# Optimization experiments

Hardware: AMD Instinct MI355X
Metric: run time of the kernel (lower is better)

The kernel has to match this reference:

```python
import jax, jax.numpy as jnp
import numpy as np
import math

B, CH, BINS, W = 2, 8, 1024, 1024
FF = 2048
BANDS = 4
HD = BINS // BANDS
EPS = 1e-5


def _ln(x, g, b):
    m = jnp.mean(x, -1, keepdims=True)
    v = jnp.mean(jnp.square(x - m), -1, keepdims=True)
    return (x - m) * jax.lax.rsqrt(v + EPS) * g + b


def _conv1d(x, w, pad, groups=1):
    # x: [B, C, W], w: [O, I/groups, k]
    return jax.lax.conv_general_dilated(x, w, (1,), [(pad, pad)],
                                        dimension_numbers=('NCH', 'OIH', 'NCH'),
                                        feature_group_count=groups)


def _attn(h, mem, qw, qb, qcw, qcb, kw, kb, kcw, kcb, vw, vb, vcw, vcb, ow, ob, er):
    b, w, c = h.shape

    def proj(src, lw, lb, cw, cb):
        y = src @ lw.T + lb                                   # [b, w, c]
        y = _conv1d(y.transpose(0, 2, 1), cw, 1, groups=c) + cb[None, :, None]
        return y.transpose(0, 2, 1)                           # [b, w, c]

    q = proj(h, qw, qb, qcw, qcb).reshape(b, w, BANDS, HD).transpose(0, 2, 1, 3)   # [b, n, w, hd]
    k = proj(mem, kw, kb, kcw, kcb).reshape(b, w, BANDS, HD).transpose(0, 2, 1, 3)
    v = proj(mem, vw, vb, vcw, vcb).reshape(b, w, BANDS, HD).transpose(0, 2, 1, 3)
    # relative position bias via Music-Transformer pad/skew trick
    p = jnp.einsum('bnwh,hc->bnwc', q, er)                    # [b, n, w, W]
    p = jnp.pad(p, ((0, 0), (0, 0), (0, 0), (1, 0))).transpose(0, 1, 3, 2)[:, :, 1:, :]
    qk = (jnp.einsum('bnqh,bnkh->bnqk', q, k) + p) / math.sqrt(c)
    a = jax.nn.softmax(qk, axis=-1)
    o = jnp.einsum('bnqk,bnkh->bnqh', a, v).transpose(0, 2, 1, 3).reshape(b, w, c)
    return o @ ow.T + ob


def _forward(x, w_in, ln1_g, ln1_b, glu_w, ln2_g, ln2_b, c1L_w, c1R_w, ln3_g, ln3_b,
             c1M_dw, c1M_pw, ln4_g, ln4_b, qw, qb, qcw, qcb, kw, kb, kcw, kcb,
             vw, vb, vcw, vcb, ow, ob, er, ln5_g, ln5_b, c2_w, c3_w):
    # in_project: Linear(channels, 1, bias=False) on x.transpose(1,3), squeeze
    xf = jnp.einsum('bcfw,c->bwf', x, w_in)                   # [B, W, BINS]
    # GLU block
    h = _ln(xf, ln1_g, ln1_b)
    g = h @ glu_w.T
    ga, gb = jnp.split(g, 2, axis=-1)
    xf = xf + ga * jax.nn.sigmoid(gb)
    # conv feedforward block
    h = _ln(xf, ln2_g, ln2_b)
    hL = jax.nn.relu(h @ c1L_w.T)                             # [B, W, FF]
    hR = jax.nn.relu(_conv1d(h.transpose(0, 2, 1), c1R_w, 1)).transpose(0, 2, 1)  # [B, W, FF//4]
    hR = jnp.pad(hR, ((0, 0), (0, 0), (0, FF - FF // 4)))
    h = _ln(hL + hR, ln3_g, ln3_b)
    h = _conv1d(_conv1d(h.transpose(0, 2, 1), c1M_dw, 4, groups=FF), c1M_pw, 0).transpose(0, 2, 1)
    xf = xf + h
    # multiband attention
    h = _ln(xf, ln4_g, ln4_b)
    h = _attn(h, h, qw, qb, qcw, qcb, kw, kb, kcw, kcb, vw, vb, vcw, vcb, ow, ob, er)
    xf = xf + h
    # squared-relu FFN
    h = _ln(xf, ln5_g, ln5_b)
    h = jnp.square(jax.nn.relu(h @ c2_w.T)) @ c3_w.T
    xf = xf + h
    return xf.transpose(0, 2, 1)[:, None, :, :]               # [B, 1, BINS, W]


def setup_inputs() -> dict:
    key = jax.random.key(0)
    keys = iter(jax.random.split(key, 48))

    def n(shape, s=0.02):
        return jax.random.normal(next(keys), shape, dtype=jnp.float32) * s

    ones = lambda d: jnp.ones((d,), jnp.float32)
    zeros = lambda d: jnp.zeros((d,), jnp.float32)
    return {
        'x': jax.random.normal(next(keys), (B, CH, BINS, W), dtype=jnp.float32),
        'w_in': n((CH,)),
        'ln1_g': ones(BINS), 'ln1_b': zeros(BINS),
        'glu_w': n((2 * BINS, BINS)),
        'ln2_g': ones(BINS), 'ln2_b': zeros(BINS),
        'c1L_w': n((FF, BINS)),
        'c1R_w': n((FF // 4, BINS, 3)),
        'ln3_g': ones(FF), 'ln3_b': zeros(FF),
        'c1M_dw': n((FF, 1, 9)),
        'c1M_pw': n((BINS, FF, 1)),
        'ln4_g': ones(BINS), 'ln4_b': zeros(BINS),
        'qw': n((BINS, BINS)), 'qb': zeros(BINS), 'qcw': n((BINS, 1, 3)), 'qcb': zeros(BINS),
        'kw': n((BINS, BINS)), 'kb': zeros(BINS), 'kcw': n((BINS, 1, 3)), 'kcb': zeros(BINS),
        'vw': n((BINS, BINS)), 'vb': zeros(BINS), 'vcw': n((BINS, 1, 3)), 'vcb': zeros(BINS),
        'ow': n((BINS, BINS)), 'ob': zeros(BINS),
        'er': n((HD, W), s=1.0),
        'ln5_g': ones(BINS), 'ln5_b': zeros(BINS),
        'c2_w': n((FF, BINS)), 'c3_w': n((BINS, FF)),
    }


def reference(x, w_in, ln1_g, ln1_b, glu_w, ln2_g, ln2_b, c1L_w, c1R_w, ln3_g, ln3_b,
              c1M_dw, c1M_pw, ln4_g, ln4_b, qw, qb, qcw, qcb, kw, kb, kcw, kcb,
              vw, vb, vcw, vcb, ow, ob, er, ln5_g, ln5_b, c2_w, c3_w):
    return _forward(x, w_in, ln1_g, ln1_b, glu_w, ln2_g, ln2_b, c1L_w, c1R_w, ln3_g, ln3_b,
                    c1M_dw, c1M_pw, ln4_g, ln4_b, qw, qb, qcw, qcb, kw, kb, kcw, kcb,
                    vw, vb, vcw, vcb, ow, ob, er, ln5_g, ln5_b, c2_w, c3_w)
```

## Files before the change

kernel.cpp:

```cpp
#include <hip/hip_runtime.h>


typedef float f32x4 __attribute__((ext_vector_type(4)));
typedef short short8 __attribute__((ext_vector_type(8)));
typedef unsigned short u16;
typedef unsigned int u32;

__device__ __forceinline__ float bf2f(u16 u){
  u32 v = ((u32)u) << 16;
  return __builtin_bit_cast(float, v);
}
__device__ __forceinline__ u16 f2bf(float f){
  u32 u = __builtin_bit_cast(u32, f);
  u32 r = (u + 0x7fffu + ((u >> 16) & 1u)) >> 16;
  return (u16)r;
}
__device__ __forceinline__ u32 pack2(float a, float b){
  return (u32)f2bf(a) | ((u32)f2bf(b) << 16);
}
__device__ __forceinline__ void unpack8(uint4 u, float* f){
  f[0]=bf2f(u.x & 0xffffu); f[1]=bf2f(u.x >> 16);
  f[2]=bf2f(u.y & 0xffffu); f[3]=bf2f(u.y >> 16);
  f[4]=bf2f(u.z & 0xffffu); f[5]=bf2f(u.z >> 16);
  f[6]=bf2f(u.w & 0xffffu); f[7]=bf2f(u.w >> 16);
}

__device__ __forceinline__ void gload16(const u16* g, u16* l){
  __builtin_amdgcn_global_load_lds(
      (const __attribute__((address_space(1))) unsigned int*)g,
      (__attribute__((address_space(3))) unsigned int*)l, 16, 0, 0);
}
template<int N> __device__ __forceinline__ void waitvm(){
  asm volatile("s_waitcnt vmcnt(%0)" :: "n"(N) : "memory");
}
__device__ __forceinline__ void barrier(){ __builtin_amdgcn_s_barrier(); }

template<int ACT, int OB, int MR, int NR, int DUAL, int NBUF, int RB, int SC>
__global__ __launch_bounds__(256)
void gemm_bt(const u16* __restrict__ A, const u16* __restrict__ Bw,
             const u16* __restrict__ A2, const u16* __restrict__ B2,
             float* __restrict__ Cf, u16* __restrict__ Cb,
             const float* __restrict__ bias, const void* __restrict__ resid,
             int M, int N, int K, int K2,
             int lda, int ldb, int lda2, int ldb2, int ldc,
             int apad, int aoff,
             long aZHi, long aZLo, long bZHi, long bZLo,
             long b2ZHi, long b2ZLo, long cZHi, long cZLo)
{
  constexpr int BM = 32 * MR, BN = 32 * NR;
  constexpr int LPT = MR + NR;
  constexpr int PRE = NBUF - 1;
  __shared__ __align__(16) u16 As[NBUF][BM * 64];
  __shared__ __align__(16) u16 Bs[NBUF][BN * 64];
  const int z = blockIdx.z, zh = z >> 2, zl = z & 3;
  const u16* Az = A + zh * aZHi + zl * aZLo;
  const u16* Bz = Bw + zh * bZHi + zl * bZLo;
  const u16* B2z = DUAL ? (B2 + zh * b2ZHi + zl * b2ZLo) : nullptr;
  const long coff = (long)zh * cZHi + (long)zl * cZLo;
  const int tid = threadIdx.x;
  const int m0 = blockIdx.y * BM, n0 = blockIdx.x * BN;
  const int lane = tid & 63, wid = tid >> 6;
  const int wm = wid >> 1, wn = wid & 1;
  const int lr = lane & 15, lk = lane >> 4;
  const int kA = K >> 6;
  const int NT = kA + (DUAL ? (K2 >> 6) : 0);

  auto stage = [&](int buf, int s){
    #pragma unroll
    for (int i = 0; i < MR; i++){
      int ch = tid + i * 256;
      int r = ch >> 3, c = ch & 7;
      int csw = (c ^ (r & 7)) * 8;
      const u16* src;
      bool d2 = DUAL && (s >= kA);
      if (d2){
        src = A2 + (long)(m0 + r) * lda2 + (s - kA) * 64 + csw;
      } else {
        int gm = m0 + r;
        long ar = (long)gm + (long)(gm >> 10) * apad + aoff;
        src = Az + ar * lda + s * 64 + csw;
      }
      gload16(src, &As[buf][ch * 8]);
    }
    #pragma unroll
    for (int i = 0; i < NR; i++){
      int ch = tid + i * 256;
      int r = ch >> 3, c = ch & 7;
      int csw = (c ^ (r & 7)) * 8;
      const u16* src;
      bool d2 = DUAL && (s >= kA);
      if (d2) src = B2z + (long)(n0 + r) * ldb2 + (s - kA) * 64 + csw;
      else    src = Bz  + (long)(n0 + r) * ldb  + s * 64 + csw;
      gload16(src, &Bs[buf][ch * 8]);
    }
  };

  f32x4 acc[MR][NR];
  #pragma unroll
  for (int i = 0; i < MR; i++)
    #pragma unroll
    for (int j = 0; j < NR; j++) acc[i][j] = f32x4{0.f, 0.f, 0.f, 0.f};

  auto compute = [&](int cur){
    const u16* Ab = &As[cur][0];
    const u16* Bb = &Bs[cur][0];
    short8 av[2][MR], bv[2][NR];
    #pragma unroll
    for (int h = 0; h < 2; h++){
      int g = h * 4 + lk;
      #pragma unroll
      for (int i = 0; i < MR; i++){
        int row = wm * 16 * MR + i * 16 + lr;
        av[h][i] = *(const short8*)(Ab + row * 64 + ((g ^ (row & 7)) * 8));
      }
      #pragma unroll
      for (int j = 0; j < NR; j++){
        int row = wn * 16 * NR + j * 16 + lr;
        bv[h][j] = *(const short8*)(Bb + row * 64 + ((g ^ (row & 7)) * 8));
      }
    }
    #pragma unroll
    for (int h = 0; h < 2; h++)
      #pragma unroll
      for (int i = 0; i < MR; i++)
        #pragma unroll
        for (int j = 0; j < NR; j++)
          acc[i][j] = __builtin_amdgcn_mfma_f32_16x16x32_bf16(av[h][i], bv[h][j], acc[i][j], 0, 0, 0);
  };

  const int npre = NT < PRE ? NT : PRE;
  for (int p = 0; p < npre; p++) stage(p, p);
  int s = 0;
  for (; s < NT - PRE; s++){
    waitvm<(NBUF - 2) * LPT>();
    barrier();
    stage((s + PRE) % NBUF, s + PRE);
    compute(s % NBUF);
    barrier();
  }
  for (; s < NT; s++){
    waitvm<0>();
    barrier();
    compute(s % NBUF);
    barrier();
  }

  float* CfZ = Cf ? Cf + coff : nullptr;
  u16*  CbZ = Cb ? Cb + coff : nullptr;
  const float* rzf = (!RB && resid) ? ((const float*)resid) + coff : nullptr;
  const u16*  rzb = (RB && resid) ? ((const u16*)resid) + coff : nullptr;
  #pragma unroll
  for (int i = 0; i < MR; i++){
    int rowb = m0 + wm * 16 * MR + i * 16 + lk * 4;
    #pragma unroll
    for (int j = 0; j < NR; j++){
      int colg = n0 + wn * 16 * NR + j * 16 + lr;
      f32x4 v = acc[i][j];
      float bvl = bias ? bias[colg] : 0.f;
      #pragma unroll
      for (int r = 0; r < 4; r++){
        long idx = (long)(rowb + r) * ldc + colg;
        float xv = v[r] + bvl;
        if constexpr (ACT == 1){ xv = fmaxf(xv, 0.f); }
        if constexpr (ACT == 2){ xv = fmaxf(xv, 0.f); xv = xv * xv; }
        if constexpr (SC){ xv *= 0.03125f; }
        if constexpr (RB){ if (rzb) xv += bf2f(rzb[idx]); }
        else             { if (rzf) xv += rzf[idx]; }
        if constexpr (OB) CbZ[idx] = f2bf(xv); else CfZ[idx] = xv;
      }
    }
  }
}

template<int NBUF>
__global__ __launch_bounds__(256)
void gemm_glu(const u16* __restrict__ A, const u16* __restrict__ Bw,
              u16* __restrict__ XF)
{
  constexpr int LPT = 6;
  constexpr int PRE = NBUF - 1;
  constexpr int NT = 16;
  __shared__ __align__(16) u16 As[NBUF][64 * 64];
  __shared__ __align__(16) u16 Bs[NBUF][128 * 64];
  const int tid = threadIdx.x;
  const int m0 = blockIdx.y * 64, n0 = blockIdx.x * 64;
  const int lane = tid & 63, wid = tid >> 6;
  const int wm = wid >> 1, wn = wid & 1;
  const int lr = lane & 15, lk = lane >> 4;

  auto stage = [&](int buf, int s){
    #pragma unroll
    for (int i = 0; i < 2; i++){
      int ch = tid + i * 256;
      int r = ch >> 3, c = ch & 7;
      int csw = (c ^ (r & 7)) * 8;
      gload16(A + (long)(m0 + r) * 1024 + s * 64 + csw, &As[buf][ch * 8]);
    }
    #pragma unroll
    for (int i = 0; i < 4; i++){
      int ch = tid + i * 256;
      int r = ch >> 3, c = ch & 7;
      int csw = (c ^ (r & 7)) * 8;
      int grow = (r < 64) ? (n0 + r) : (1024 + n0 + r - 64);
      gload16(Bw + (long)grow * 1024 + s * 64 + csw, &Bs[buf][ch * 8]);
    }
  };

  f32x4 accv[2][2], accg[2][2];
  #pragma unroll
  for (int i = 0; i < 2; i++)
    #pragma unroll
    for (int j = 0; j < 2; j++){
      accv[i][j] = f32x4{0.f,0.f,0.f,0.f};
      accg[i][j] = f32x4{0.f,0.f,0.f,0.f};
    }

  auto compute = [&](int cur){
    const u16* Ab = &As[cur][0];
    const u16* Bb = &Bs[cur][0];
    short8 av[2][2], bvv[2][2], bvg[2][2];
    #pragma unroll
    for (int h = 0; h < 2; h++){
      int g = h * 4 + lk;
      #pragma unroll
      for (int i = 0; i < 2; i++){
        int row = wm * 32 + i * 16 + lr;
        av[h][i] = *(const short8*)(Ab + row * 64 + ((g ^ (row & 7)) * 8));
      }
      #pragma unroll
      for (int j = 0; j < 2; j++){
        int row = wn * 32 + j * 16 + lr;
        bvv[h][j] = *(const short8*)(Bb + row * 64 + ((g ^ (row & 7)) * 8));
        int rowg = 64 + row;
        bvg[h][j] = *(const short8*)(Bb + rowg * 64 + ((g ^ (rowg & 7)) * 8));
      }
    }
    #pragma unroll
    for (int h = 0; h < 2; h++)
      #pragma unroll
      for (int i = 0; i < 2; i++)
        #pragma unroll
        for (int j = 0; j < 2; j++){
          accv[i][j] = __builtin_amdgcn_mfma_f32_16x16x32_bf16(av[h][i], bvv[h][j], accv[i][j], 0, 0, 0);
          accg[i][j] = __builtin_amdgcn_mfma_f32_16x16x32_bf16(av[h][i], bvg[h][j], accg[i][j], 0, 0, 0);
        }
  };

  const int npre = NT < PRE ? NT : PRE;
  for (int p = 0; p < npre; p++) stage(p, p);
  int s = 0;
  for (; s < NT - PRE; s++){
    waitvm<(NBUF - 2) * LPT>();
    barrier();
    stage((s + PRE) % NBUF, s + PRE);
    compute(s % NBUF);
    barrier();
  }
  for (; s < NT; s++){
    waitvm<0>();
    barrier();
    compute(s % NBUF);
    barrier();
  }

  #pragma unroll
  for (int i = 0; i < 2; i++){
    int rowb = m0 + wm * 32 + i * 16 + lk * 4;
    #pragma unroll
    for (int j = 0; j < 2; j++){
      int colg = n0 + wn * 32 + j * 16 + lr;
      #pragma unroll
      for (int r = 0; r < 4; r++){
        long idx = (long)(rowb + r) * 1024 + colg;
        float g = accg[i][j][r];
        float nv = bf2f(XF[idx]) + accv[i][j][r] / (1.f + __expf(-g));
        XF[idx] = f2bf(nv);
      }
    }
  }
}

template<int NC, int INBF>
__global__ __launch_bounds__(256)
void ln_kernel(const void* __restrict__ in, u16* __restrict__ out,
               const float* __restrict__ gg, const float* __restrict__ bb,
               int rowpad, int rowadd)
{
  constexpr int PER = NC / 256;
  const int row = blockIdx.x;
  const int tid = threadIdx.x;
  float v[PER];
  if constexpr (INBF){
    const u16* x = ((const u16*)in) + (long)row * NC + tid * PER;
    if constexpr (PER == 4){
      uint2 u = *(const uint2*)x;
      v[0]=bf2f(u.x & 0xffffu); v[1]=bf2f(u.x >> 16);
      v[2]=bf2f(u.y & 0xffffu); v[3]=bf2f(u.y >> 16);
    } else {
      #pragma unroll
      for (int i = 0; i < PER; i += 8){
        uint4 u = *(const uint4*)(x + i);
        unpack8(u, &v[i]);
      }
    }
  } else {
    const float* x = ((const float*)in) + (long)row * NC + tid * PER;
    #pragma unroll
    for (int i = 0; i < PER; i += 4){
      f32x4 t = *(const f32x4*)(x + i);
      v[i] = t.x; v[i+1] = t.y; v[i+2] = t.z; v[i+3] = t.w;
    }
  }
  float s = 0.f, sq = 0.f;
  #pragma unroll
  for (int i = 0; i < PER; i++){ s += v[i]; sq += v[i] * v[i]; }
  #pragma unroll
  for (int o = 32; o; o >>= 1){ s += __shfl_xor(s, o); sq += __shfl_xor(sq, o); }
  __shared__ float as_[4], aq_[4];
  const int wv = tid >> 6;
  if ((tid & 63) == 0){ as_[wv] = s; aq_[wv] = sq; }
  __syncthreads();
  s  = as_[0] + as_[1] + as_[2] + as_[3];
  sq = aq_[0] + aq_[1] + aq_[2] + aq_[3];
  const float mean = s * (1.f / NC);
  const float var  = sq * (1.f / NC) - mean * mean;
  const float rs = rsqrtf(var + 1e-5f);
  const long orow = (long)row + (long)(row >> 10) * rowpad + rowadd;
  u16* op = out + orow * NC + tid * PER;
  u32 word[PER / 2];
  #pragma unroll
  for (int i = 0; i < PER; i += 2){
    int c = tid * PER + i;
    float y0 = (v[i]   - mean) * rs * gg[c]   + bb[c];
    float y1 = (v[i+1] - mean) * rs * gg[c+1] + bb[c+1];
    word[i / 2] = pack2(y0, y1);
  }
  if constexpr (PER == 4) *(uint2*)op = *(uint2*)word;
  else                    *(uint4*)op = *(uint4*)word;
}

__global__ __launch_bounds__(256)
void inproj_kernel(const float* __restrict__ x, const float* __restrict__ w_in,
                   u16* __restrict__ xf)
{
  __shared__ float tile[32][33];
  const int b = blockIdx.z, f0 = blockIdx.x * 32, w0 = blockIdx.y * 32;
  const int tx = threadIdx.x, ty = threadIdx.y;
  float wr[8];
  #pragma unroll
  for (int c = 0; c < 8; c++) wr[c] = w_in[c];
  #pragma unroll
  for (int i = 0; i < 4; i++){
    int f = f0 + ty + i * 8;
    float s = 0.f;
    #pragma unroll
    for (int c = 0; c < 8; c++)
      s += x[(((long)(b * 8 + c)) * 1024 + f) * 1024 + w0 + tx] * wr[c];
    tile[ty + i * 8][tx] = s;
  }
  __syncthreads();
  #pragma unroll
  for (int i = 0; i < 4; i++){
    int wl = ty + i * 8;
    xf[((long)(b * 1024 + w0 + wl)) * 1024 + f0 + tx] = f2bf(tile[tx][wl]);
  }
}

__global__ __launch_bounds__(256)
void tr_out_kernel(const u16* __restrict__ xf, float* __restrict__ out)
{
  __shared__ float tile[32][33];
  const int b = blockIdx.z, f0 = blockIdx.x * 32, w0 = blockIdx.y * 32;
  const int tx = threadIdx.x, ty = threadIdx.y;
  #pragma unroll
  for (int i = 0; i < 4; i++)
    tile[ty + i * 8][tx] = bf2f(xf[((long)(b * 1024 + w0 + ty + i * 8)) * 1024 + f0 + tx]);
  __syncthreads();
  #pragma unroll
  for (int i = 0; i < 4; i++)
    out[((long)(b * 1024 + f0 + ty + i * 8)) * 1024 + w0 + tx] = tile[tx][ty + i * 8];
}

__global__ __launch_bounds__(256)
void dwconv9_kernel(const u16* __restrict__ in, u16* __restrict__ out,
                    const float* __restrict__ dwT)
{
  const int id = blockIdx.x * 256 + threadIdx.x;
  const int cg = id & 255;
  const int tg = id >> 8;
  const int c0 = cg * 8;
  const int t0 = tg * 4;
  const int b = t0 >> 10;
  const int w0 = t0 & 1023;
  const u16* bin = in + ((long)b << 10) * 2048 + c0;
  float wt[9][8];
  #pragma unroll
  for (int j = 0; j < 9; j++){
    f32x4 lo = *(const f32x4*)(dwT + j * 2048 + c0);
    f32x4 hi = *(const f32x4*)(dwT + j * 2048 + c0 + 4);
    wt[j][0]=lo.x; wt[j][1]=lo.y; wt[j][2]=lo.z; wt[j][3]=lo.w;
    wt[j][4]=hi.x; wt[j][5]=hi.y; wt[j][6]=hi.z; wt[j][7]=hi.w;
  }
  float win[9][8];
  #pragma unroll
  for (int r = 0; r < 9; r++){
    int wr = w0 - 4 + r;
    if (wr >= 0 && wr < 1024){
      uint4 u = *(const uint4*)(bin + (long)wr * 2048);
      unpack8(u, win[r]);
    } else {
      #pragma unroll
      for (int i = 0; i < 8; i++) win[r][i] = 0.f;
    }
  }
  #pragma unroll
  for (int s = 0; s < 4; s++){
    float acc[8] = {0,0,0,0,0,0,0,0};
    #pragma unroll
    for (int j = 0; j < 9; j++)
      #pragma unroll
      for (int i = 0; i < 8; i++)
        acc[i] += win[(s + j) % 9][i] * wt[j][i];
    uint4 o;
    o.x = pack2(acc[0], acc[1]); o.y = pack2(acc[2], acc[3]);
    o.z = pack2(acc[4], acc[5]); o.w = pack2(acc[6], acc[7]);
    *(uint4*)(out + (long)(t0 + s) * 2048 + c0) = o;
    if (s < 3){
      int wr = w0 + s + 5;
      if (wr < 1024){
        uint4 u = *(const uint4*)(bin + (long)wr * 2048);
        unpack8(u, win[s % 9]);
      } else {
        #pragma unroll
        for (int i = 0; i < 8; i++) win[s % 9][i] = 0.f;
      }
    }
  }
}

__global__ __launch_bounds__(256)
void conv3_kernel(const u16* __restrict__ qin, u16* __restrict__ qout,
                  const float* __restrict__ qwT, const float* __restrict__ qbb,
                  const u16* __restrict__ kin, u16* __restrict__ kout,
                  const float* __restrict__ kwT, const float* __restrict__ kbb,
                  int ld)
{
  const int sel = blockIdx.y;
  const u16* in  = sel ? kin : qin;
  u16* out       = sel ? kout : qout;
  const float* wT = sel ? kwT : qwT;
  const float* bp = sel ? kbb : qbb;
  const int id = blockIdx.x * 256 + threadIdx.x;
  const int cg = id & 127;
  const int tg = id >> 7;
  const int c0 = cg * 8;
  const int t0 = tg * 4;
  const int b = t0 >> 10;
  const int w0 = t0 & 1023;
  const u16* bin = in + ((long)b << 10) * ld + c0;
  float wt[3][8], bias[8];
  #pragma unroll
  for (int j = 0; j < 3; j++){
    f32x4 lo = *(const f32x4*)(wT + j * 1024 + c0);
    f32x4 hi = *(const f32x4*)(wT + j * 1024 + c0 + 4);
    wt[j][0]=lo.x; wt[j][1]=lo.y; wt[j][2]=lo.z; wt[j][3]=lo.w;
    wt[j][4]=hi.x; wt[j][5]=hi.y; wt[j][6]=hi.z; wt[j][7]=hi.w;
  }
  {
    f32x4 lo = *(const f32x4*)(bp + c0);
    f32x4 hi = *(const f32x4*)(bp + c0 + 4);
    bias[0]=lo.x; bias[1]=lo.y; bias[2]=lo.z; bias[3]=lo.w;
    bias[4]=hi.x; bias[5]=hi.y; bias[6]=hi.z; bias[7]=hi.w;
  }
  float win[3][8];
  #pragma unroll
  for (int r = 0; r < 3; r++){
    int wr = w0 - 1 + r;
    if (wr >= 0 && wr < 1024){
      uint4 u = *(const uint4*)(bin + (long)wr * ld);
      unpack8(u, win[r]);
    } else {
      #pragma unroll
      for (int i = 0; i < 8; i++) win[r][i] = 0.f;
    }
  }
  #pragma unroll
  for (int s = 0; s < 4; s++){
    float acc[8];
    #pragma unroll
    for (int i = 0; i < 8; i++) acc[i] = bias[i];
    #pragma unroll
    for (int j = 0; j < 3; j++)
      #pragma unroll
      for (int i = 0; i < 8; i++)
        acc[i] += win[(s + j) % 3][i] * wt[j][i];
    uint4 o;
    o.x = pack2(acc[0], acc[1]); o.y = pack2(acc[2], acc[3]);
    o.z = pack2(acc[4], acc[5]); o.w = pack2(acc[6], acc[7]);
    *(uint4*)(out + (long)(t0 + s) * 1024 + c0) = o;
    if (s < 3){
      int wr = w0 + s + 2;
      if (wr < 1024){
        uint4 u = *(const uint4*)(bin + (long)wr * ld);
        unpack8(u, win[s % 3]);
      } else {
        #pragma unroll
        for (int i = 0; i < 8; i++) win[s % 3][i] = 0.f;
      }
    }
  }
}

__global__ __launch_bounds__(256)
void vconv3t_kernel(const u16* __restrict__ in, u16* __restrict__ out,
                    const float* __restrict__ cw, const float* __restrict__ cb,
                    int ld)
{
  __shared__ float ins[34][33];
  __shared__ float outs[32][33];
  const int b = blockIdx.z, w0 = blockIdx.x * 32, c0 = blockIdx.y * 32;
  const int tx = threadIdx.x, ty = threadIdx.y;
  for (int r = ty; r < 34; r += 8){
    int w = w0 - 1 + r;
    ins[r][tx] = (w >= 0 && w < 1024) ? bf2f(in[((long)(b * 1024 + w)) * ld + c0 + tx]) : 0.f;
  }
  __syncthreads();
  const float wt0 = cw[(c0 + tx) * 3 + 0], wt1 = cw[(c0 + tx) * 3 + 1], wt2 = cw[(c0 + tx) * 3 + 2];
  const float bb = cb[c0 + tx];
  #pragma unroll
  for (int i = 0; i < 4; i++){
    int wl = ty + i * 8;
    outs[wl][tx] = ins[wl][tx] * wt0 + ins[wl + 1][tx] * wt1 + ins[wl + 2][tx] * wt2 + bb;
  }
  __syncthreads();
  #pragma unroll
  for (int i = 0; i < 4; i++){
    int cl = ty + i * 8;
    int c = c0 + cl; int n = c >> 8; int h = c & 255;
    out[((long)((b * 4 + n) * 256 + h)) * 1024 + w0 + tx] = f2bf(outs[tx][cl]);
  }
}

__global__ __launch_bounds__(256)
void softmax_kernel(u16* __restrict__ buf)
{
  const long row = blockIdx.x;
  const int tid = threadIdx.x;
  u16* p = buf + row * 1024 + tid * 4;
  uint2 u = *(const uint2*)p;
  float v0 = bf2f(u.x & 0xffffu), v1 = bf2f(u.x >> 16);
  float v2 = bf2f(u.y & 0xffffu), v3 = bf2f(u.y >> 16);
  float m = fmaxf(fmaxf(v0, v1), fmaxf(v2, v3));
  #pragma unroll
  for (int o = 32; o; o >>= 1) m = fmaxf(m, __shfl_xor(m, o));
  __shared__ float sm[4], ssum[4];
  const int wv = tid >> 6;
  if ((tid & 63) == 0) sm[wv] = m;
  __syncthreads();
  m = fmaxf(fmaxf(sm[0], sm[1]), fmaxf(sm[2], sm[3]));
  float e0 = __expf(v0 - m), e1 = __expf(v1 - m);
  float e2 = __expf(v2 - m), e3 = __expf(v3 - m);
  float s = e0 + e1 + e2 + e3;
  #pragma unroll
  for (int o = 32; o; o >>= 1) s += __shfl_xor(s, o);
  if ((tid & 63) == 0) ssum[wv] = s;
  __syncthreads();
  s = ssum[0] + ssum[1] + ssum[2] + ssum[3];
  const float inv = 1.f / s;
  uint2 o2;
  o2.x = pack2(e0 * inv, e1 * inv);
  o2.y = pack2(e2 * inv, e3 * inv);
  *(uint2*)p = o2;
}

struct Ptrs9 { const float* s[9]; u16* d[9]; };

__global__ __launch_bounds__(256)
void prep_cvt_kernel(Ptrs9 p)
{
  constexpr int n4s[9] = {524288,524288,524288,262144,262144,262144,262144,524288,524288};
  const int job = blockIdx.y;
  const int id = blockIdx.x * 256 + threadIdx.x;
  if (id >= n4s[job]) return;
  f32x4 v = *(const f32x4*)(p.s[job] + (long)id * 4);
  uint2 o; o.x = pack2(v.x, v.y); o.y = pack2(v.z, v.w);
  *(uint2*)(p.d[job] + (long)id * 4) = o;
}

__global__ __launch_bounds__(256)
void prep_misc_kernel(const float* __restrict__ c1R_w, u16* __restrict__ wb_c1R,
                      const float* __restrict__ er, u16* __restrict__ wb_erT,
                      const float* __restrict__ c1M_dw, float* __restrict__ dwT,
                      const float* __restrict__ qcw, float* __restrict__ qcwT,
                      const float* __restrict__ kcw, float* __restrict__ kcwT,
                      const float* __restrict__ qb, const float* __restrict__ kb,
                      const float* __restrict__ vb, float* __restrict__ bqkv,
                      u16* __restrict__ hpad)
{
  const int bid = blockIdx.x;
  const int tid = threadIdx.x;
  if (bid < 6144){
    int id = bid * 256 + tid;
    int oc = id / 3072; int rem = id - oc * 3072;
    int tau = rem >> 10; int ic = rem & 1023;
    wb_c1R[id] = f2bf(c1R_w[(long)oc * 3072 + ic * 3 + tau]);
  } else if (bid < 7168){
    int id = (bid - 6144) * 256 + tid;
    int qi = id >> 8; int h = id & 255;
    wb_erT[id] = f2bf(er[(long)h * 1024 + qi]);
  } else if (bid < 7240){
    int id = (bid - 7168) * 256 + tid;
    int jj = id >> 11; int c = id & 2047;
    dwT[id] = c1M_dw[c * 9 + jj];
  } else if (bid < 7252){
    int id = (bid - 7240) * 256 + tid;
    int jj = id >> 10; int c = id & 1023;
    qcwT[id] = qcw[c * 3 + jj];
  } else if (bid < 7264){
    int id = (bid - 7252) * 256 + tid;
    int jj = id >> 10; int c = id & 1023;
    kcwT[id] = kcw[c * 3 + jj];
  } else if (bid < 7276){
    int id = (bid - 7264) * 256 + tid;
    bqkv[id] = (id < 1024) ? qb[id] : (id < 2048) ? kb[id - 1024] : vb[id - 2048];
  } else {
    int id = (bid - 7276) * 256 + tid;
    int r = id >> 10; int c = id & 1023;
    int b = r >> 1; int edge = r & 1;
    long row = (long)b * 1026 + (edge ? 1025 : 0);
    hpad[row * 1024 + c] = 0;
  }
}

extern "C" void kernel_launch(void* const* d_in, const int* in_sizes, int n_in,
                              void* d_out, int out_size, void* d_ws, size_t ws_size,
                              hipStream_t stream)
{
  (void)in_sizes; (void)n_in; (void)out_size; (void)ws_size;
  const float* x     = (const float*)d_in[0];
  const float* w_in  = (const float*)d_in[1];
  const float* ln1_g = (const float*)d_in[2];
  const float* ln1_b = (const float*)d_in[3];
  const float* glu_w = (const float*)d_in[4];
  const float* ln2_g = (const float*)d_in[5];
  const float* ln2_b = (const float*)d_in[6];
  const float* c1L_w = (const float*)d_in[7];
  const float* c1R_w = (const float*)d_in[8];
  const float* ln3_g = (const float*)d_in[9];
  const float* ln3_b = (const float*)d_in[10];
  const float* c1M_dw= (const float*)d_in[11];
  const float* c1M_pw= (const float*)d_in[12];
  const float* ln4_g = (const float*)d_in[13];
  const float* ln4_b = (const float*)d_in[14];
  const float* qw  = (const float*)d_in[15];
  const float* qb  = (const float*)d_in[16];
  const float* qcw = (const float*)d_in[17];
  const float* qcb = (const float*)d_in[18];
  const float* kw  = (const float*)d_in[19];
  const float* kb  = (const float*)d_in[20];
  const float* kcw = (const float*)d_in[21];
  const float* kcb = (const float*)d_in[22];
  const float* vw  = (const float*)d_in[23];
  const float* vb  = (const float*)d_in[24];
  const float* vcw = (const float*)d_in[25];
  const float* vcb = (const float*)d_in[26];
  const float* ow  = (const float*)d_in[27];
  const float* ob  = (const float*)d_in[28];
  const float* er  = (const float*)d_in[29];
  const float* ln5_g = (const float*)d_in[30];
  const float* ln5_b = (const float*)d_in[31];
  const float* c2_w  = (const float*)d_in[32];
  const float* c3_w  = (const float*)d_in[33];
  float* out = (float*)d_out;

  const long TT = 2048;
  char* wsb = (char*)d_ws;
  size_t off = 0;
  auto alloc = [&](size_t bytes) -> char* {
    char* p = wsb + off;
    off = (off + bytes + 255) & ~(size_t)255;
    return p;
  };
  u16* XF     = (u16*)alloc(TT * 1024 * 2);
  u16* wb_glu = (u16*)alloc(2048L * 1024 * 2);
  u16* wb_c1L = (u16*)alloc(2048L * 1024 * 2);
  u16* wb_c1R = (u16*)alloc(512L * 3072 * 2);
  u16* wb_pw  = (u16*)alloc(1024L * 2048 * 2);
  u16* wb_q   = (u16*)alloc(1024L * 1024 * 2);
  u16* wb_k   = (u16*)alloc(1024L * 1024 * 2);
  u16* wb_v   = (u16*)alloc(1024L * 1024 * 2);
  u16* wb_ow  = (u16*)alloc(1024L * 1024 * 2);
  u16* wb_c2  = (u16*)alloc(2048L * 1024 * 2);
  u16* wb_c3  = (u16*)alloc(1024L * 2048 * 2);
  u16* wb_erT = (u16*)alloc(1024L * 256 * 2);
  float* dwT  = (float*)alloc(9L * 2048 * 4);
  float* qcwT = (float*)alloc(3L * 1024 * 4);
  float* kcwT = (float*)alloc(3L * 1024 * 4);
  float* bqkv = (float*)alloc(3072L * 4);
  u16* HPAD   = (u16*)alloc(2L * 1026 * 1024 * 2);
  u16* LNA    = (u16*)alloc(TT * 1024 * 2);
  u16* HS     = (u16*)alloc(TT * 2048 * 2);
  u16* LN3O   = (u16*)alloc(TT * 2048 * 2);
  u16* DW9O   = (u16*)alloc(TT * 2048 * 2);
  u16* SBF    = (u16*)alloc(8L * 1024 * 1024 * 2);
  u16* qkvbuf = (u16*)alloc(TT * 3072 * 2);
  u16* q2b  = (u16*)alloc(TT * 1024 * 2);
  u16* k2b  = (u16*)alloc(TT * 1024 * 2);
  u16* v2T  = (u16*)alloc(8L * 256 * 1024 * 2);
  u16* obuf = qkvbuf;
  u16* C2O  = LN3O;

  Ptrs9 pj;
  pj.s[0]=glu_w; pj.d[0]=wb_glu;
  pj.s[1]=c1L_w; pj.d[1]=wb_c1L;
  pj.s[2]=c1M_pw; pj.d[2]=wb_pw;
  pj.s[3]=qw; pj.d[3]=wb_q;
  pj.s[4]=kw; pj.d[4]=wb_k;
  pj.s[5]=vw; pj.d[5]=wb_v;
  pj.s[6]=ow; pj.d[6]=wb_ow;
  pj.s[7]=c2_w; pj.d[7]=wb_c2;
  pj.s[8]=c3_w; pj.d[8]=wb_c3;
  prep_cvt_kernel<<<dim3(2048, 9), 256, 0, stream>>>(pj);
  prep_misc_kernel<<<7292, 256, 0, stream>>>(c1R_w, wb_c1R, er, wb_erT, c1M_dw, dwT,
                                             qcw, qcwT, kcw, kcwT, qb, kb, vb, bqkv, HPAD);

  inproj_kernel<<<dim3(32, 32, 2), dim3(32, 8), 0, stream>>>(x, w_in, XF);

  ln_kernel<1024,1><<<2048, 256, 0, stream>>>(XF, LNA, ln1_g, ln1_b, 0, 0);
  gemm_glu<3><<<dim3(16,32,1), 256, 0, stream>>>(LNA, wb_glu, XF);

  ln_kernel<1024,1><<<2048, 256, 0, stream>>>(XF, HPAD, ln2_g, ln2_b, 2, 1);
  gemm_bt<1,1,4,2,0,3,0,0><<<dim3(32,16,1), 256, 0, stream>>>(HPAD, wb_c1L, nullptr, nullptr,
      nullptr, HS, nullptr, nullptr,
      2048, 2048, 1024, 0, 1024, 1024, 0, 0, 2048, 2, 1, 0,0,0,0,0,0,0,0);
  gemm_bt<1,1,2,2,0,4,1,0><<<dim3(8,32,1), 256, 0, stream>>>(HPAD, wb_c1R, nullptr, nullptr,
      nullptr, HS, nullptr, HS,
      2048, 512, 3072, 0, 1024, 3072, 0, 0, 2048, 2, 0, 0,0,0,0,0,0,0,0);
  ln_kernel<2048,1><<<2048, 256, 0, stream>>>(HS, LN3O, ln3_g, ln3_b, 0, 0);
  dwconv9_kernel<<<512, 256, 0, stream>>>(LN3O, DW9O, dwT);
  gemm_bt<0,1,2,2,0,3,1,0><<<dim3(16,32,1), 256, 0, stream>>>(DW9O, wb_pw, nullptr, nullptr,
      nullptr, XF, nullptr, XF,
      2048, 1024, 2048, 0, 2048, 2048, 0, 0, 1024, 0, 0, 0,0,0,0,0,0,0,0);

  ln_kernel<1024,1><<<2048, 256, 0, stream>>>(XF, LNA, ln4_g, ln4_b, 0, 0);
  gemm_bt<0,1,4,2,0,3,0,0><<<dim3(48,16,1), 256, 0, stream>>>(LNA, wb_q, nullptr, nullptr,
      nullptr, qkvbuf, bqkv, nullptr,
      2048, 3072, 1024, 0, 1024, 1024, 0, 0, 3072, 0, 0, 0,0,0,0,0,0,0,0);
  conv3_kernel<<<dim3(256,2), 256, 0, stream>>>(qkvbuf, q2b, qcwT, qcb,
                                                qkvbuf + 1024, k2b, kcwT, kcb, 3072);
  vconv3t_kernel<<<dim3(32, 32, 2), dim3(32, 8), 0, stream>>>(qkvbuf + 2048, v2T, vcw, vcb, 3072);
  gemm_bt<0,1,4,2,1,3,0,1><<<dim3(16,8,8), 256, 0, stream>>>(q2b, k2b, wb_erT, q2b,
      nullptr, SBF, nullptr, nullptr,
      1024, 1024, 256, 256, 1024, 1024, 256, 1024, 1024, 0, 0,
      1048576, 256, 1048576, 256, 1048576, 256, 4194304, 1048576);
  softmax_kernel<<<8192, 256, 0, stream>>>(SBF);
  gemm_bt<0,1,2,2,0,3,0,0><<<dim3(4,16,8), 256, 0, stream>>>(SBF, v2T, nullptr, nullptr,
      nullptr, obuf, nullptr, nullptr,
      1024, 256, 1024, 0, 1024, 1024, 0, 0, 1024, 0, 0,
      4194304, 1048576, 1048576, 262144, 0, 0, 1048576, 256);
  gemm_bt<0,1,2,2,0,3,1,0><<<dim3(16,32,1), 256, 0, stream>>>(obuf, wb_ow, nullptr, nullptr,
      nullptr, XF, ob, XF,
      2048, 1024, 1024, 0, 1024, 1024, 0, 0, 1024, 0, 0, 0,0,0,0,0,0,0,0);

  ln_kernel<1024,1><<<2048, 256, 0, stream>>>(XF, LNA, ln5_g, ln5_b, 0, 0);
  gemm_bt<2,1,4,2,0,3,0,0><<<dim3(32,16,1), 256, 0, stream>>>(LNA, wb_c2, nullptr, nullptr,
      nullptr, C2O, nullptr, nullptr,
      2048, 2048, 1024, 0, 1024, 1024, 0, 0, 2048, 0, 0, 0,0,0,0,0,0,0,0);
  gemm_bt<0,1,2,2,0,3,1,0><<<dim3(16,32,1), 256, 0, stream>>>(C2O, wb_c3, nullptr, nullptr,
      nullptr, XF, nullptr, XF,
      2048, 1024, 2048, 0, 2048, 2048, 0, 0, 1024, 0, 0, 0,0,0,0,0,0,0,0);

  tr_out_kernel<<<dim3(32, 32, 2), dim3(32, 8), 0, stream>>>(XF, out);
}
```

Measured before the change: 331.1 us.

## Drop trailing GEMM barriers, merge prep and qkv conv kernels, retune pipeline depth

Removes the trailing barrier after each compute step in the GEMM main loops, relying on the leading barrier plus multi-buffering to avoid LDS overwrite hazards. Merges the two weight-prep kernels into one launch and the q/k and v depthwise-conv kernels into one launch to cut launch overhead. Lowers a pipeline-depth template parameter from 3 to 2 for several GEMMs, which changes prefetch distance and LDS use. Removing barriers risks a race if the stage distance leaves no free buffer slot.

```diff
diff --git a/kernel.cpp b/kernel.cpp
--- a/kernel.cpp
+++ b/kernel.cpp
@@ -136,13 +136,11 @@
     barrier();
     stage((s + PRE) % NBUF, s + PRE);
     compute(s % NBUF);
-    barrier();
   }
   for (; s < NT; s++){
     waitvm<0>();
     barrier();
     compute(s % NBUF);
-    barrier();
   }
 
   float* CfZ = Cf ? Cf + coff : nullptr;
@@ -254,13 +252,11 @@
     barrier();
     stage((s + PRE) % NBUF, s + PRE);
     compute(s % NBUF);
-    barrier();
   }
   for (; s < NT; s++){
     waitvm<0>();
     barrier();
     compute(s % NBUF);
-    barrier();
   }
 
   #pragma unroll
@@ -439,105 +435,106 @@
 }
 
 __global__ __launch_bounds__(256)
-void conv3_kernel(const u16* __restrict__ qin, u16* __restrict__ qout,
-                  const float* __restrict__ qwT, const float* __restrict__ qbb,
-                  const u16* __restrict__ kin, u16* __restrict__ kout,
-                  const float* __restrict__ kwT, const float* __restrict__ kbb,
-                  int ld)
-{
-  const int sel = blockIdx.y;
-  const u16* in  = sel ? kin : qin;
-  u16* out       = sel ? kout : qout;
-  const float* wT = sel ? kwT : qwT;
-  const float* bp = sel ? kbb : qbb;
-  const int id = blockIdx.x * 256 + threadIdx.x;
-  const int cg = id & 127;
-  const int tg = id >> 7;
-  const int c0 = cg * 8;
-  const int t0 = tg * 4;
-  const int b = t0 >> 10;
-  const int w0 = t0 & 1023;
-  const u16* bin = in + ((long)b << 10) * ld + c0;
-  float wt[3][8], bias[8];
-  #pragma unroll
-  for (int j = 0; j < 3; j++){
-    f32x4 lo = *(const f32x4*)(wT + j * 1024 + c0);
-    f32x4 hi = *(const f32x4*)(wT + j * 1024 + c0 + 4);
-    wt[j][0]=lo.x; wt[j][1]=lo.y; wt[j][2]=lo.z; wt[j][3]=lo.w;
-    wt[j][4]=hi.x; wt[j][5]=hi.y; wt[j][6]=hi.z; wt[j][7]=hi.w;
-  }
-  {
-    f32x4 lo = *(const f32x4*)(bp + c0);
-    f32x4 hi = *(const f32x4*)(bp + c0 + 4);
-    bias[0]=lo.x; bias[1]=lo.y; bias[2]=lo.z; bias[3]=lo.w;
-    bias[4]=hi.x; bias[5]=hi.y; bias[6]=hi.z; bias[7]=hi.w;
-  }
-  float win[3][8];
-  #pragma unroll
-  for (int r = 0; r < 3; r++){
-    int wr = w0 - 1 + r;
-    if (wr >= 0 && wr < 1024){
-      uint4 u = *(const uint4*)(bin + (long)wr * ld);
-      unpack8(u, win[r]);
-    } else {
-      #pragma unroll
-      for (int i = 0; i < 8; i++) win[r][i] = 0.f;
-    }
-  }
-  #pragma unroll
-  for (int s = 0; s < 4; s++){
-    float acc[8];
-    #pragma unroll
-    for (int i = 0; i < 8; i++) acc[i] = bias[i];
-    #pragma unroll
-    for (int j = 0; j < 3; j++)
-      #pragma unroll
-      for (int i = 0; i < 8; i++)
-        acc[i] += win[(s + j) % 3][i] * wt[j][i];
-    uint4 o;
-    o.x = pack2(acc[0], acc[1]); o.y = pack2(acc[2], acc[3]);
-    o.z = pack2(acc[4], acc[5]); o.w = pack2(acc[6], acc[7]);
-    *(uint4*)(out + (long)(t0 + s) * 1024 + c0) = o;
-    if (s < 3){
-      int wr = w0 + s + 2;
-      if (wr < 1024){
-        uint4 u = *(const uint4*)(bin + (long)wr * ld);
-        unpack8(u, win[s % 3]);
+void qkvconv_kernel(const u16* __restrict__ qkv,
+                    u16* __restrict__ q2b, const float* __restrict__ qwT, const float* __restrict__ qbb,
+                    u16* __restrict__ k2b, const float* __restrict__ kwT, const float* __restrict__ kbb,
+                    u16* __restrict__ v2T, const float* __restrict__ vcw, const float* __restrict__ vcb)
+{
+  __shared__ float ins[34][33];
+  __shared__ float outs[32][33];
+  const int bid = blockIdx.x;
+  const int tid = threadIdx.x;
+  if (bid < 512){
+    const int sel = bid >> 8;
+    const u16* in  = qkv + sel * 1024;
+    u16* out       = sel ? k2b : q2b;
+    const float* wT = sel ? kwT : qwT;
+    const float* bp = sel ? kbb : qbb;
+    const int id = (bid & 255) * 256 + tid;
+    const int cg = id & 127;
+    const int tg = id >> 7;
+    const int c0 = cg * 8;
+    const int t0 = tg * 4;
+    const int b = t0 >> 10;
+    const int w0 = t0 & 1023;
+    const u16* bin = in + ((long)b << 10) * 3072 + c0;
+    float wt[3][8], bias[8];
+    #pragma unroll
+    for (int j = 0; j < 3; j++){
+      f32x4 lo = *(const f32x4*)(wT + j * 1024 + c0);
+      f32x4 hi = *(const f32x4*)(wT + j * 1024 + c0 + 4);
+      wt[j][0]=lo.x; wt[j][1]=lo.y; wt[j][2]=lo.z; wt[j][3]=lo.w;
+      wt[j][4]=hi.x; wt[j][5]=hi.y; wt[j][6]=hi.z; wt[j][7]=hi.w;
+    }
+    {
+      f32x4 lo = *(const f32x4*)(bp + c0);
+      f32x4 hi = *(const f32x4*)(bp + c0 + 4);
+      bias[0]=lo.x; bias[1]=lo.y; bias[2]=lo.z; bias[3]=lo.w;
+      bias[4]=hi.x; bias[5]=hi.y; bias[6]=hi.z; bias[7]=hi.w;
+    }
+    float win[3][8];
+    #pragma unroll
+    for (int r = 0; r < 3; r++){
+      int wr = w0 - 1 + r;
+      if (wr >= 0 && wr < 1024){
+        uint4 u = *(const uint4*)(bin + (long)wr * 3072);
+        unpack8(u, win[r]);
       } else {
         #pragma unroll
-        for (int i = 0; i < 8; i++) win[s % 3][i] = 0.f;
-      }
-    }
-  }
-}
-
-__global__ __launch_bounds__(256)
-void vconv3t_kernel(const u16* __restrict__ in, u16* __restrict__ out,
-                    const float* __restrict__ cw, const float* __restrict__ cb,
-                    int ld)
-{
-  __shared__ float ins[34][33];
-  __shared__ float outs[32][33];
-  const int b = blockIdx.z, w0 = blockIdx.x * 32, c0 = blockIdx.y * 32;
-  const int tx = threadIdx.x, ty = threadIdx.y;
-  for (int r = ty; r < 34; r += 8){
-    int w = w0 - 1 + r;
-    ins[r][tx] = (w >= 0 && w < 1024) ? bf2f(in[((long)(b * 1024 + w)) * ld + c0 + tx]) : 0.f;
-  }
-  __syncthreads();
-  const float wt0 = cw[(c0 + tx) * 3 + 0], wt1 = cw[(c0 + tx) * 3 + 1], wt2 = cw[(c0 + tx) * 3 + 2];
-  const float bb = cb[c0 + tx];
-  #pragma unroll
-  for (int i = 0; i < 4; i++){
-    int wl = ty + i * 8;
-    outs[wl][tx] = ins[wl][tx] * wt0 + ins[wl + 1][tx] * wt1 + ins[wl + 2][tx] * wt2 + bb;
-  }
-  __syncthreads();
-  #pragma unroll
-  for (int i = 0; i < 4; i++){
-    int cl = ty + i * 8;
-    int c = c0 + cl; int n = c >> 8; int h = c & 255;
-    out[((long)((b * 4 + n) * 256 + h)) * 1024 + w0 + tx] = f2bf(outs[tx][cl]);
+        for (int i = 0; i < 8; i++) win[r][i] = 0.f;
+      }
+    }
+    #pragma unroll
+    for (int s = 0; s < 4; s++){
+      float acc[8];
+      #pragma unroll
+      for (int i = 0; i < 8; i++) acc[i] = bias[i];
+      #pragma unroll
+      for (int j = 0; j < 3; j++)
+        #pragma unroll
+        for (int i = 0; i < 8; i++)
+          acc[i] += win[(s + j) % 3][i] * wt[j][i];
+      uint4 o;
+      o.x = pack2(acc[0], acc[1]); o.y = pack2(acc[2], acc[3]);
+      o.z = pack2(acc[4], acc[5]); o.w = pack2(acc[6], acc[7]);
+      *(uint4*)(out + (long)(t0 + s) * 1024 + c0) = o;
+      if (s < 3){
+        int wr = w0 + s + 2;
+        if (wr < 1024){
+          uint4 u = *(const uint4*)(bin + (long)wr * 3072);
+          unpack8(u, win[s % 3]);
+        } else {
+          #pragma unroll
+          for (int i = 0; i < 8; i++) win[s % 3][i] = 0.f;
+        }
+      }
+    }
+  } else {
+    const int vb = bid - 512;
+    const int b = vb >> 10;
+    const int rem = vb & 1023;
+    const int w0 = (rem & 31) * 32, c0 = (rem >> 5) * 32;
+    const int tx = tid & 31, ty = tid >> 5;
+    const u16* in = qkv + 2048;
+    for (int r = ty; r < 34; r += 8){
+      int w = w0 - 1 + r;
+      ins[r][tx] = (w >= 0 && w < 1024) ? bf2f(in[((long)(b * 1024 + w)) * 3072 + c0 + tx]) : 0.f;
+    }
+    __syncthreads();
+    const float wt0 = vcw[(c0 + tx) * 3 + 0], wt1 = vcw[(c0 + tx) * 3 + 1], wt2 = vcw[(c0 + tx) * 3 + 2];
+    const float bb = vcb[c0 + tx];
+    #pragma unroll
+    for (int i = 0; i < 4; i++){
+      int wl = ty + i * 8;
+      outs[wl][tx] = ins[wl][tx] * wt0 + ins[wl + 1][tx] * wt1 + ins[wl + 2][tx] * wt2 + bb;
+    }
+    __syncthreads();
+    #pragma unroll
+    for (int i = 0; i < 4; i++){
+      int cl = ty + i * 8;
+      int c = c0 + cl; int n = c >> 8; int h = c & 255;
+      v2T[((long)((b * 4 + n) * 256 + h)) * 1024 + w0 + tx] = f2bf(outs[tx][cl]);
+    }
   }
 }
 
@@ -576,29 +573,28 @@
 struct Ptrs9 { const float* s[9]; u16* d[9]; };
 
 __global__ __launch_bounds__(256)
-void prep_cvt_kernel(Ptrs9 p)
+void prep_all_kernel(Ptrs9 p,
+                     const float* __restrict__ c1R_w, u16* __restrict__ wb_c1R,
+                     const float* __restrict__ er, u16* __restrict__ wb_erT,
+                     const float* __restrict__ c1M_dw, float* __restrict__ dwT,
+                     const float* __restrict__ qcw, float* __restrict__ qcwT,
+                     const float* __restrict__ kcw, float* __restrict__ kcwT,
+                     const float* __restrict__ qb, const float* __restrict__ kb,
+                     const float* __restrict__ vb, float* __restrict__ bqkv,
+                     u16* __restrict__ hpad)
 {
   constexpr int n4s[9] = {524288,524288,524288,262144,262144,262144,262144,524288,524288};
-  const int job = blockIdx.y;
-  const int id = blockIdx.x * 256 + threadIdx.x;
-  if (id >= n4s[job]) return;
-  f32x4 v = *(const f32x4*)(p.s[job] + (long)id * 4);
-  uint2 o; o.x = pack2(v.x, v.y); o.y = pack2(v.z, v.w);
-  *(uint2*)(p.d[job] + (long)id * 4) = o;
-}
-
-__global__ __launch_bounds__(256)
-void prep_misc_kernel(const float* __restrict__ c1R_w, u16* __restrict__ wb_c1R,
-                      const float* __restrict__ er, u16* __restrict__ wb_erT,
-                      const float* __restrict__ c1M_dw, float* __restrict__ dwT,
-                      const float* __restrict__ qcw, float* __restrict__ qcwT,
-                      const float* __restrict__ kcw, float* __restrict__ kcwT,
-                      const float* __restrict__ qb, const float* __restrict__ kb,
-                      const float* __restrict__ vb, float* __restrict__ bqkv,
-                      u16* __restrict__ hpad)
-{
-  const int bid = blockIdx.x;
   const int tid = threadIdx.x;
+  if (blockIdx.x < 18432){
+    const int job = blockIdx.x >> 11;
+    const int id = (blockIdx.x & 2047) * 256 + tid;
+    if (id >= n4s[job]) return;
+    f32x4 v = *(const f32x4*)(p.s[job] + (long)id * 4);
+    uint2 o; o.x = pack2(v.x, v.y); o.y = pack2(v.z, v.w);
+    *(uint2*)(p.d[job] + (long)id * 4) = o;
+    return;
+  }
+  const int bid = blockIdx.x - 18432;
   if (bid < 6144){
     int id = bid * 256 + tid;
     int oc = id / 3072; int rem = id - oc * 3072;
@@ -720,17 +716,16 @@
   pj.s[6]=ow; pj.d[6]=wb_ow;
   pj.s[7]=c2_w; pj.d[7]=wb_c2;
   pj.s[8]=c3_w; pj.d[8]=wb_c3;
-  prep_cvt_kernel<<<dim3(2048, 9), 256, 0, stream>>>(pj);
-  prep_misc_kernel<<<7292, 256, 0, stream>>>(c1R_w, wb_c1R, er, wb_erT, c1M_dw, dwT,
+  prep_all_kernel<<<25724, 256, 0, stream>>>(pj, c1R_w, wb_c1R, er, wb_erT, c1M_dw, dwT,
                                              qcw, qcwT, kcw, kcwT, qb, kb, vb, bqkv, HPAD);
 
   inproj_kernel<<<dim3(32, 32, 2), dim3(32, 8), 0, stream>>>(x, w_in, XF);
 
   ln_kernel<1024,1><<<2048, 256, 0, stream>>>(XF, LNA, ln1_g, ln1_b, 0, 0);
-  gemm_glu<3><<<dim3(16,32,1), 256, 0, stream>>>(LNA, wb_glu, XF);
+  gemm_glu<2><<<dim3(16,32,1), 256, 0, stream>>>(LNA, wb_glu, XF);
 
   ln_kernel<1024,1><<<2048, 256, 0, stream>>>(XF, HPAD, ln2_g, ln2_b, 2, 1);
-  gemm_bt<1,1,4,2,0,3,0,0><<<dim3(32,16,1), 256, 0, stream>>>(HPAD, wb_c1L, nullptr, nullptr,
+  gemm_bt<1,1,4,2,0,2,0,0><<<dim3(32,16,1), 256, 0, stream>>>(HPAD, wb_c1L, nullptr, nullptr,
       nullptr, HS, nullptr, nullptr,
       2048, 2048, 1024, 0, 1024, 1024, 0, 0, 2048, 2, 1, 0,0,0,0,0,0,0,0);
   gemm_bt<1,1,2,2,0,4,1,0><<<dim3(8,32,1), 256, 0, stream>>>(HPAD, wb_c1R, nullptr, nullptr,
@@ -743,13 +738,12 @@
       2048, 1024, 2048, 0, 2048, 2048, 0, 0, 1024, 0, 0, 0,0,0,0,0,0,0,0);
 
   ln_kernel<1024,1><<<2048, 256, 0, stream>>>(XF, LNA, ln4_g, ln4_b, 0, 0);
-  gemm_bt<0,1,4,2,0,3,0,0><<<dim3(48,16,1), 256, 0, stream>>>(LNA, wb_q, nullptr, nullptr,
+  gemm_bt<0,1,4,2,0,2,0,0><<<dim3(48,16,1), 256, 0, stream>>>(LNA, wb_q, nullptr, nullptr,
       nullptr, qkvbuf, bqkv, nullptr,
       2048, 3072, 1024, 0, 1024, 1024, 0, 0, 3072, 0, 0, 0,0,0,0,0,0,0,0);
-  conv3_kernel<<<dim3(256,2), 256, 0, stream>>>(qkvbuf, q2b, qcwT, qcb,
-                                                qkvbuf + 1024, k2b, kcwT, kcb, 3072);
-  vconv3t_kernel<<<dim3(32, 32, 2), dim3(32, 8), 0, stream>>>(qkvbuf + 2048, v2T, vcw, vcb, 3072);
-  gemm_bt<0,1,4,2,1,3,0,1><<<dim3(16,8,8), 256, 0, stream>>>(q2b, k2b, wb_erT, q2b,
+  qkvconv_kernel<<<2560, 256, 0, stream>>>(qkvbuf, q2b, qcwT, qcb, k2b, kcwT, kcb,
+                                           v2T, vcw, vcb);
+  gemm_bt<0,1,4,2,1,2,0,1><<<dim3(16,8,8), 256, 0, stream>>>(q2b, k2b, wb_erT, q2b,
       nullptr, SBF, nullptr, nullptr,
       1024, 1024, 256, 256, 1024, 1024, 256, 1024, 1024, 0, 0,
       1048576, 256, 1048576, 256, 1048576, 256, 4194304, 1048576);
@@ -763,7 +757,7 @@
       2048, 1024, 1024, 0, 1024, 1024, 0, 0, 1024, 0, 0, 0,0,0,0,0,0,0,0);
 
   ln_kernel<1024,1><<<2048, 256, 0, stream>>>(XF, LNA, ln5_g, ln5_b, 0, 0);
-  gemm_bt<2,1,4,2,0,3,0,0><<<dim3(32,16,1), 256, 0, stream>>>(LNA, wb_c2, nullptr, nullptr,
+  gemm_bt<2,1,4,2,0,2,0,0><<<dim3(32,16,1), 256, 0, stream>>>(LNA, wb_c2, nullptr, nullptr,
       nullptr, C2O, nullptr, nullptr,
       2048, 2048, 1024, 0, 1024, 1024, 0, 0, 2048, 0, 0, 0,0,0,0,0,0,0,0);
   gemm_bt<0,1,2,2,0,3,1,0><<<dim3(16,32,1), 256, 0, stream>>>(C2O, wb_c3, nullptr, nullptr,
```

Measured after the change: 300.8 us. 1.1x faster.
